# Performance work log

Hardware: AMD Instinct MI355X
Metric: run time of the kernel (lower is better)

## Reference

```python
import jax, jax.numpy as jnp
import numpy as np

N_NODES = 50000
N_EDGES = 800000
IN_C, HID_C, OUT_C = 256, 256, 128


def gcn_conv(x, W, b, row, col, n_nodes):
    """PyG GCNConv: linear transform, symmetric-normalized aggregation, bias.
    row/col already include self-loops. Messages flow row -> col."""
    h = x @ W  # [N, out]
    deg = jax.ops.segment_sum(jnp.ones_like(col, dtype=h.dtype), col, num_segments=n_nodes)
    d_inv_sqrt = jnp.where(deg > 0, jax.lax.rsqrt(jnp.maximum(deg, 1e-12)), 0.0)
    norm = d_inv_sqrt[row] * d_inv_sqrt[col]  # [E]
    msg = h[row] * norm[:, None]              # gather + scale, [E, out]
    out = jax.ops.segment_sum(msg, col, num_segments=n_nodes)  # scatter-add
    return out + b


def setup_inputs() -> dict:
    key = jax.random.key(0)
    k_x, k_e, k_w1, k_w2 = jax.random.split(key, 4)
    x = jax.random.normal(k_x, (N_NODES, IN_C), dtype=jnp.float32)
    edge_index = jax.random.randint(k_e, (2, N_EDGES), 0, N_NODES, dtype=jnp.int64)
    # Glorot-style init for GCN weights, zeros bias (PyG default)
    s1 = float(np.sqrt(6.0 / (IN_C + HID_C)))
    s2 = float(np.sqrt(6.0 / (HID_C + OUT_C)))
    W1 = jax.random.uniform(k_w1, (IN_C, HID_C), dtype=jnp.float32, minval=-s1, maxval=s1)
    b1 = jnp.zeros((HID_C,), dtype=jnp.float32)
    W2 = jax.random.uniform(k_w2, (HID_C, OUT_C), dtype=jnp.float32, minval=-s2, maxval=s2)
    b2 = jnp.zeros((OUT_C,), dtype=jnp.float32)
    return {"x": x, "edge_index": edge_index, "W1": W1, "b1": b1, "W2": W2, "b2": b2}


def reference(x, edge_index, W1, b1, W2, b2):
    n = x.shape[0]
    # add self-loops (PyG GCNConv default add_self_loops=True)
    loops = jnp.arange(n, dtype=edge_index.dtype)
    row = jnp.concatenate([edge_index[0], loops])
    col = jnp.concatenate([edge_index[1], loops])
    h = gcn_conv(x, W1, b1, row, col, n)
    h = jax.nn.relu(h)  # dropout p=0.0 -> identity
    out = gcn_conv(h, W2, b2, row, col, n)
    return out
```

## Files before the change

### kernel.cpp

```cpp
#include <hip/hip_runtime.h>

#define NN 50000
#define NE 800000
#define IN_C 256
#define HID_C 256
#define OUT_C 128

typedef unsigned short u16;
typedef __attribute__((ext_vector_type(8))) short short8;
typedef __attribute__((ext_vector_type(8))) unsigned short ushort8;
typedef __attribute__((ext_vector_type(4))) float f32x4;

__device__ __forceinline__ u16 f2b(float f) {
  unsigned int u = __float_as_uint(f);
  return (u16)((u + 0x7FFFu + ((u >> 16) & 1u)) >> 16);
}
__device__ __forceinline__ float b2f(u16 s) {
  return __uint_as_float(((unsigned int)s) << 16);
}


__global__ __launch_bounds__(256) void hist_kernel(const int* __restrict__ col,
                                                   int* __restrict__ cnt, int E) {
  int e = blockIdx.x * blockDim.x + threadIdx.x;
  if (e < E) atomicAdd(&cnt[col[e]], 1);
}

__global__ __launch_bounds__(256) void scan1_kernel(const int* __restrict__ cnt,
                                                    int* __restrict__ bsum, int n) {
  __shared__ int ws[4];
  int i = blockIdx.x * 256 + threadIdx.x;
  int lane = threadIdx.x & 63, wid = threadIdx.x >> 6;
  int v = (i < n) ? cnt[i] : 0;
#pragma unroll
  for (int off = 32; off > 0; off >>= 1) v += __shfl_down(v, off, 64);
  if (lane == 0) ws[wid] = v;
  __syncthreads();
  if (threadIdx.x == 0) bsum[blockIdx.x] = ws[0] + ws[1] + ws[2] + ws[3];
}

__global__ __launch_bounds__(256) void scan2_kernel(const int* __restrict__ bsum,
                                                    int* __restrict__ boff,
                                                    int* __restrict__ row_off,
                                                    int nb, int n) {
  __shared__ int wsum[4], wpre[5];
  int lane = threadIdx.x & 63, wid = threadIdx.x >> 6;
  int v = (threadIdx.x < nb) ? bsum[threadIdx.x] : 0;
  int s = v;
#pragma unroll
  for (int off = 1; off < 64; off <<= 1) {
    int t = __shfl_up(s, off, 64);
    if (lane >= off) s += t;
  }
  if (lane == 63) wsum[wid] = s;
  __syncthreads();
  if (threadIdx.x == 0) {
    int acc = 0;
#pragma unroll
    for (int w = 0; w < 4; ++w) { wpre[w] = acc; acc += wsum[w]; }
    wpre[4] = acc;
  }
  __syncthreads();
  if (threadIdx.x < nb) boff[threadIdx.x] = wpre[wid] + (s - v);
  if (threadIdx.x == 0) row_off[n] = wpre[4];
}

__global__ __launch_bounds__(256) void scan3_kernel(const int* __restrict__ cnt,
                                                    const int* __restrict__ boff,
                                                    int* __restrict__ row_off,
                                                    int* __restrict__ cursor,
                                                    float* __restrict__ dinv, int n) {
  __shared__ int wsum[4], wpre[4];
  int i = blockIdx.x * 256 + threadIdx.x;
  int lane = threadIdx.x & 63, wid = threadIdx.x >> 6;
  int v = (i < n) ? cnt[i] : 0;
  int s = v;
#pragma unroll
  for (int off = 1; off < 64; off <<= 1) {
    int t = __shfl_up(s, off, 64);
    if (lane >= off) s += t;
  }
  if (lane == 63) wsum[wid] = s;
  __syncthreads();
  if (threadIdx.x == 0) {
    int acc = 0;
#pragma unroll
    for (int w = 0; w < 4; ++w) { wpre[w] = acc; acc += wsum[w]; }
  }
  __syncthreads();
  if (i < n) {
    int off = boff[blockIdx.x] + wpre[wid] + (s - v);
    row_off[i] = off;
    cursor[i] = off;
    dinv[i] = rsqrtf((float)(v + 1));
  }
}

__global__ __launch_bounds__(256) void scatter_kernel(const int* __restrict__ row,
                                                      const int* __restrict__ col,
                                                      const float* __restrict__ dinv,
                                                      int* __restrict__ cursor,
                                                      int2* __restrict__ csr, int E) {
  int e = blockIdx.x * blockDim.x + threadIdx.x;
  if (e < E) {
    int r = row[e], c = col[e];
    int p = atomicAdd(&cursor[c], 1);
    csr[p] = make_int2(r, __float_as_int(dinv[r] * dinv[c]));
  }
}


__global__ __launch_bounds__(256) void convw_kernel(const float* __restrict__ W1,
                                                    const float* __restrict__ W2,
                                                    u16* __restrict__ W1t,
                                                    u16* __restrict__ W2t) {
  int id = blockIdx.x * 256 + threadIdx.x;
  if (id < 256 * 256) {
    int n = id >> 8, k = id & 255;
    W1t[id] = f2b(W1[k * 256 + n]);
  }
  if (id < 128 * 256) {
    int n = id >> 8, k = id & 255;
    W2t[id] = f2b(W2[k * 128 + n]);
  }
}


template <bool A_IS_F32>
__global__ __launch_bounds__(256) void gemm_mfma(const void* __restrict__ Ap,
                                                 const u16* __restrict__ Bt,
                                                 u16* __restrict__ C, int M, int N) {
  __shared__ u16 Asl[2][128 * 40];
  __shared__ u16 Bsl[2][128 * 40];
  const int tid = threadIdx.x;
  const int row0 = blockIdx.y * 128;
  const int col0 = blockIdx.x * 128;

  f32x4 acc[4][4] = {};

  const int seg = tid & 7;
  const int rb = tid >> 3;
  const int wave = tid >> 6, lane = tid & 63;
  const int wm = wave >> 1, wn = wave & 1;
  const int qr = lane & 15, quad = lane >> 4;

  float4 aF[4];
  ushort4 aU[4];
  ushort4 bR[4];

  auto load_tiles = [&](int k0) {
    if constexpr (A_IS_F32) {
      const float* A = (const float*)Ap;
#pragma unroll
      for (int i = 0; i < 4; ++i) {
        int gr = row0 + rb + i * 32;
        aF[i] = (gr < M) ? *(const float4*)&A[(size_t)gr * 256 + k0 + seg * 4]
                         : make_float4(0.f, 0.f, 0.f, 0.f);
      }
    } else {
      const u16* A = (const u16*)Ap;
#pragma unroll
      for (int i = 0; i < 4; ++i) {
        int gr = row0 + rb + i * 32;
        aU[i] = (gr < M) ? *(const ushort4*)&A[(size_t)gr * 256 + k0 + seg * 4]
                         : make_ushort4(0, 0, 0, 0);
      }
    }
#pragma unroll
    for (int i = 0; i < 4; ++i) {
      int n = rb + i * 32;
      bR[i] = *(const ushort4*)&Bt[(size_t)(col0 + n) * 256 + k0 + seg * 4];
    }
  };

  auto write_lds = [&](int buf) {
#pragma unroll
    for (int i = 0; i < 4; ++i) {
      int r = rb + i * 32;
      ushort4 u;
      if constexpr (A_IS_F32) {
        u.x = f2b(aF[i].x); u.y = f2b(aF[i].y);
        u.z = f2b(aF[i].z); u.w = f2b(aF[i].w);
      } else {
        u = aU[i];
      }
      *(ushort4*)&Asl[buf][r * 40 + seg * 4] = u;
      *(ushort4*)&Bsl[buf][r * 40 + seg * 4] = bR[i];
    }
  };

  load_tiles(0);
  write_lds(0);
  __syncthreads();

#pragma unroll
  for (int it = 0; it < 8; ++it) {
    const int cur = it & 1;
    if (it < 7) load_tiles((it + 1) * 32);

    short8 afr[4], bfr[4];
#pragma unroll
    for (int mt = 0; mt < 4; ++mt)
      afr[mt] = *(const short8*)&Asl[cur][(wm * 64 + mt * 16 + qr) * 40 + quad * 8];
#pragma unroll
    for (int nt = 0; nt < 4; ++nt)
      bfr[nt] = *(const short8*)&Bsl[cur][(wn * 64 + nt * 16 + qr) * 40 + quad * 8];
#pragma unroll
    for (int mt = 0; mt < 4; ++mt)
#pragma unroll
      for (int nt = 0; nt < 4; ++nt)
        acc[mt][nt] = __builtin_amdgcn_mfma_f32_16x16x32_bf16(afr[mt], bfr[nt], acc[mt][nt], 0, 0, 0);

    if (it < 7) {
      write_lds(1 - cur);
      __syncthreads();
    }
  }

#pragma unroll
  for (int mt = 0; mt < 4; ++mt) {
#pragma unroll
    for (int nt = 0; nt < 4; ++nt) {
      int gc = col0 + wn * 64 + nt * 16 + qr;
#pragma unroll
      for (int i = 0; i < 4; ++i) {
        int gr = row0 + wm * 64 + mt * 16 + quad * 4 + i;
        if (gr < M) C[(size_t)gr * N + gc] = f2b(acc[mt][nt][i]);
      }
    }
  }
}


__global__ __launch_bounds__(256) void agg256_bf(const u16* __restrict__ h,
                                                 const int* __restrict__ row_off,
                                                 const int2* __restrict__ csr,
                                                 const float* __restrict__ dinv,
                                                 const float* __restrict__ bias,
                                                 u16* __restrict__ out, int n) {
  int wave = threadIdx.x >> 6;
  int lane = threadIdx.x & 63;
  int half = lane >> 5;
  int sl = lane & 31;
  int v = blockIdx.x * 8 + wave * 2 + half;
  if (v >= n) return;
  int beg = row_off[v], end = row_off[v + 1];
  float a[8] = {};
  int e = beg;
  for (; e + 3 < end; e += 4) {
    int2 e0 = csr[e], e1 = csr[e + 1], e2 = csr[e + 2], e3 = csr[e + 3];
    ushort8 h0 = *(const ushort8*)&h[(size_t)e0.x * 256 + sl * 8];
    ushort8 h1 = *(const ushort8*)&h[(size_t)e1.x * 256 + sl * 8];
    ushort8 h2 = *(const ushort8*)&h[(size_t)e2.x * 256 + sl * 8];
    ushort8 h3 = *(const ushort8*)&h[(size_t)e3.x * 256 + sl * 8];
    float w0 = __int_as_float(e0.y), w1 = __int_as_float(e1.y);
    float w2 = __int_as_float(e2.y), w3 = __int_as_float(e3.y);
#pragma unroll
    for (int i = 0; i < 8; ++i)
      a[i] += b2f((u16)h0[i]) * w0 + b2f((u16)h1[i]) * w1 +
              b2f((u16)h2[i]) * w2 + b2f((u16)h3[i]) * w3;
  }
  for (; e < end; ++e) {
    int2 e0 = csr[e];
    ushort8 h0 = *(const ushort8*)&h[(size_t)e0.x * 256 + sl * 8];
    float w0 = __int_as_float(e0.y);
#pragma unroll
    for (int i = 0; i < 8; ++i) a[i] += b2f((u16)h0[i]) * w0;
  }
  float dv = dinv[v];
  float sw = dv * dv;
  ushort8 hs = *(const ushort8*)&h[(size_t)v * 256 + sl * 8];
  float4 bv0 = *(const float4*)&bias[sl * 8];
  float4 bv1 = *(const float4*)&bias[sl * 8 + 4];
  float bb[8] = {bv0.x, bv0.y, bv0.z, bv0.w, bv1.x, bv1.y, bv1.z, bv1.w};
  ushort8 o;
#pragma unroll
  for (int i = 0; i < 8; ++i) {
    float r = fmaxf(a[i] + b2f((u16)hs[i]) * sw + bb[i], 0.f);
    o[i] = (short)f2b(r);
  }
  *(ushort8*)&out[(size_t)v * 256 + sl * 8] = o;
}

__global__ __launch_bounds__(256) void agg128_bf(const u16* __restrict__ h,
                                                 const int* __restrict__ row_off,
                                                 const int2* __restrict__ csr,
                                                 const float* __restrict__ dinv,
                                                 const float* __restrict__ bias,
                                                 float* __restrict__ out, int n) {
  int wave = threadIdx.x >> 6;
  int lane = threadIdx.x & 63;
  int quarter = lane >> 4;
  int sl = lane & 15;
  int v = blockIdx.x * 16 + wave * 4 + quarter;
  if (v >= n) return;
  int beg = row_off[v], end = row_off[v + 1];
  float a[8] = {};
  int e = beg;
  for (; e + 3 < end; e += 4) {
    int2 e0 = csr[e], e1 = csr[e + 1], e2 = csr[e + 2], e3 = csr[e + 3];
    ushort8 h0 = *(const ushort8*)&h[(size_t)e0.x * 128 + sl * 8];
    ushort8 h1 = *(const ushort8*)&h[(size_t)e1.x * 128 + sl * 8];
    ushort8 h2 = *(const ushort8*)&h[(size_t)e2.x * 128 + sl * 8];
    ushort8 h3 = *(const ushort8*)&h[(size_t)e3.x * 128 + sl * 8];
    float w0 = __int_as_float(e0.y), w1 = __int_as_float(e1.y);
    float w2 = __int_as_float(e2.y), w3 = __int_as_float(e3.y);
#pragma unroll
    for (int i = 0; i < 8; ++i)
      a[i] += b2f((u16)h0[i]) * w0 + b2f((u16)h1[i]) * w1 +
              b2f((u16)h2[i]) * w2 + b2f((u16)h3[i]) * w3;
  }
  for (; e < end; ++e) {
    int2 e0 = csr[e];
    ushort8 h0 = *(const ushort8*)&h[(size_t)e0.x * 128 + sl * 8];
    float w0 = __int_as_float(e0.y);
#pragma unroll
    for (int i = 0; i < 8; ++i) a[i] += b2f((u16)h0[i]) * w0;
  }
  float dv = dinv[v];
  float sw = dv * dv;
  ushort8 hs = *(const ushort8*)&h[(size_t)v * 128 + sl * 8];
  float4 bv0 = *(const float4*)&bias[sl * 8];
  float4 bv1 = *(const float4*)&bias[sl * 8 + 4];
  float bb[8] = {bv0.x, bv0.y, bv0.z, bv0.w, bv1.x, bv1.y, bv1.z, bv1.w};
  float o[8];
#pragma unroll
  for (int i = 0; i < 8; ++i) o[i] = a[i] + b2f((u16)hs[i]) * sw + bb[i];
  *(float4*)&out[(size_t)v * 128 + sl * 8] = make_float4(o[0], o[1], o[2], o[3]);
  *(float4*)&out[(size_t)v * 128 + sl * 8 + 4] = make_float4(o[4], o[5], o[6], o[7]);
}


extern "C" void kernel_launch(void* const* d_in, const int* in_sizes, int n_in,
                              void* d_out, int out_size, void* d_ws, size_t ws_size,
                              hipStream_t stream) {
  const float* x = (const float*)d_in[0];
  const int* ei = (const int*)d_in[1];
  const float* W1 = (const float*)d_in[2];
  const float* b1 = (const float*)d_in[3];
  const float* W2 = (const float*)d_in[4];
  const float* b2 = (const float*)d_in[5];
  float* out = (float*)d_out;

  const int* row = ei;
  const int* col = ei + NE;

  const int NB = (NN + 255) / 256;

  u16* Hb = (u16*)d_ws;
  u16* H2b = Hb + (size_t)NN * 256;
  u16* H3b = H2b + (size_t)NN * 256;
  u16* W1t = H3b + (size_t)NN * 128;
  u16* W2t = W1t + 256 * 256;
  int* cnt = (int*)(W2t + 128 * 256);
  int* row_off = cnt + NN;
  int* cursor = row_off + NN + 1;
  float* dinv = (float*)(cursor + NN);
  int* bsum = (int*)(dinv + NN);
  int* boff = bsum + NB;
  int2* csr = (int2*)(boff + NB);

  hipMemsetAsync(cnt, 0, NN * sizeof(int), stream);
  convw_kernel<<<256, 256, 0, stream>>>(W1, W2, W1t, W2t);
  hist_kernel<<<(NE + 255) / 256, 256, 0, stream>>>(col, cnt, NE);
  scan1_kernel<<<NB, 256, 0, stream>>>(cnt, bsum, NN);
  scan2_kernel<<<1, 256, 0, stream>>>(bsum, boff, row_off, NB, NN);
  scan3_kernel<<<NB, 256, 0, stream>>>(cnt, boff, row_off, cursor, dinv, NN);
  scatter_kernel<<<(NE + 255) / 256, 256, 0, stream>>>(row, col, dinv, cursor, csr, NE);

  {
    dim3 grid(HID_C / 128, (NN + 127) / 128);
    gemm_mfma<true><<<grid, 256, 0, stream>>>(x, W1t, Hb, NN, HID_C);
  }
  agg256_bf<<<(NN + 7) / 8, 256, 0, stream>>>(Hb, row_off, csr, dinv, b1, H2b, NN);

  {
    dim3 grid(OUT_C / 128, (NN + 127) / 128);
    gemm_mfma<false><<<grid, 256, 0, stream>>>(H2b, W2t, H3b, NN, OUT_C);
  }
  agg128_bf<<<(NN + 15) / 16, 256, 0, stream>>>(H3b, row_off, csr, dinv, b2, out, NN);
}
```

Measured before the change: 307.7 us.

## Fold symmetric normalization into GEMM epilogue and store source-only CSR

The d^-1/2 factor of the source node is now applied to each row in the GEMM epilogue, and the destination factor is applied once per node after aggregation. The CSR therefore holds only source indices (int instead of int2), and the aggregation loop becomes a plain sum. That loop is also unrolled to 8 gathers in flight to expose more memory parallelism. This halves CSR traffic and removes per-edge multiplies, at the cost of a per-row dinv load in the GEMM epilogue and more registers in the aggregation kernels.

```diff
diff --git a/kernel.cpp b/kernel.cpp
--- a/kernel.cpp
+++ b/kernel.cpp
@@ -98,14 +98,13 @@
 
 __global__ __launch_bounds__(256) void scatter_kernel(const int* __restrict__ row,
                                                       const int* __restrict__ col,
-                                                      const float* __restrict__ dinv,
                                                       int* __restrict__ cursor,
-                                                      int2* __restrict__ csr, int E) {
+                                                      int* __restrict__ csr, int E) {
   int e = blockIdx.x * blockDim.x + threadIdx.x;
   if (e < E) {
-    int r = row[e], c = col[e];
+    int c = col[e];
     int p = atomicAdd(&cursor[c], 1);
-    csr[p] = make_int2(r, __float_as_int(dinv[r] * dinv[c]));
+    csr[p] = row[e];
   }
 }
 
@@ -129,6 +128,7 @@
 template <bool A_IS_F32>
 __global__ __launch_bounds__(256) void gemm_mfma(const void* __restrict__ Ap,
                                                  const u16* __restrict__ Bt,
+                                                 const float* __restrict__ dscale,
                                                  u16* __restrict__ C, int M, int N) {
   __shared__ u16 Asl[2][128 * 40];
   __shared__ u16 Bsl[2][128 * 40];
@@ -220,12 +220,15 @@
 #pragma unroll
   for (int mt = 0; mt < 4; ++mt) {
 #pragma unroll
-    for (int nt = 0; nt < 4; ++nt) {
-      int gc = col0 + wn * 64 + nt * 16 + qr;
-#pragma unroll
-      for (int i = 0; i < 4; ++i) {
-        int gr = row0 + wm * 64 + mt * 16 + quad * 4 + i;
-        if (gr < M) C[(size_t)gr * N + gc] = f2b(acc[mt][nt][i]);
+    for (int i = 0; i < 4; ++i) {
+      int gr = row0 + wm * 64 + mt * 16 + quad * 4 + i;
+      if (gr < M) {
+        float sc = dscale[gr];
+#pragma unroll
+        for (int nt = 0; nt < 4; ++nt) {
+          int gc = col0 + wn * 64 + nt * 16 + qr;
+          C[(size_t)gr * N + gc] = f2b(acc[mt][nt][i] * sc);
+        }
       }
     }
   }
@@ -234,7 +237,7 @@
 
 __global__ __launch_bounds__(256) void agg256_bf(const u16* __restrict__ h,
                                                  const int* __restrict__ row_off,
-                                                 const int2* __restrict__ csr,
+                                                 const int* __restrict__ csr,
                                                  const float* __restrict__ dinv,
                                                  const float* __restrict__ bias,
                                                  u16* __restrict__ out, int n) {
@@ -247,36 +250,43 @@
   int beg = row_off[v], end = row_off[v + 1];
   float a[8] = {};
   int e = beg;
-  for (; e + 3 < end; e += 4) {
-    int2 e0 = csr[e], e1 = csr[e + 1], e2 = csr[e + 2], e3 = csr[e + 3];
-    ushort8 h0 = *(const ushort8*)&h[(size_t)e0.x * 256 + sl * 8];
-    ushort8 h1 = *(const ushort8*)&h[(size_t)e1.x * 256 + sl * 8];
-    ushort8 h2 = *(const ushort8*)&h[(size_t)e2.x * 256 + sl * 8];
-    ushort8 h3 = *(const ushort8*)&h[(size_t)e3.x * 256 + sl * 8];
-    float w0 = __int_as_float(e0.y), w1 = __int_as_float(e1.y);
-    float w2 = __int_as_float(e2.y), w3 = __int_as_float(e3.y);
-#pragma unroll
-    for (int i = 0; i < 8; ++i)
-      a[i] += b2f((u16)h0[i]) * w0 + b2f((u16)h1[i]) * w1 +
-              b2f((u16)h2[i]) * w2 + b2f((u16)h3[i]) * w3;
-  }
-  for (; e < end; ++e) {
-    int2 e0 = csr[e];
-    ushort8 h0 = *(const ushort8*)&h[(size_t)e0.x * 256 + sl * 8];
-    float w0 = __int_as_float(e0.y);
-#pragma unroll
-    for (int i = 0; i < 8; ++i) a[i] += b2f((u16)h0[i]) * w0;
-  }
+  for (; e + 7 < end; e += 8) {
+    int s[8];
+#pragma unroll
+    for (int j = 0; j < 8; ++j) s[j] = csr[e + j];
+    ushort8 g[8];
+#pragma unroll
+    for (int j = 0; j < 8; ++j)
+      g[j] = *(const ushort8*)&h[(size_t)s[j] * 256 + sl * 8];
+#pragma unroll
+    for (int j = 0; j < 8; ++j)
+#pragma unroll
+      for (int i = 0; i < 8; ++i) a[i] += b2f((u16)g[j][i]);
+  }
+  for (; e + 1 < end; e += 2) {
+    int s0 = csr[e], s1 = csr[e + 1];
+    ushort8 g0 = *(const ushort8*)&h[(size_t)s0 * 256 + sl * 8];
+    ushort8 g1 = *(const ushort8*)&h[(size_t)s1 * 256 + sl * 8];
+#pragma unroll
+    for (int i = 0; i < 8; ++i) a[i] += b2f((u16)g0[i]) + b2f((u16)g1[i]);
+  }
+  if (e < end) {
+    int s0 = csr[e];
+    ushort8 g0 = *(const ushort8*)&h[(size_t)s0 * 256 + sl * 8];
+#pragma unroll
+    for (int i = 0; i < 8; ++i) a[i] += b2f((u16)g0[i]);
+  }
+  ushort8 hs = *(const ushort8*)&h[(size_t)v * 256 + sl * 8];
+#pragma unroll
+  for (int i = 0; i < 8; ++i) a[i] += b2f((u16)hs[i]);
   float dv = dinv[v];
-  float sw = dv * dv;
-  ushort8 hs = *(const ushort8*)&h[(size_t)v * 256 + sl * 8];
   float4 bv0 = *(const float4*)&bias[sl * 8];
   float4 bv1 = *(const float4*)&bias[sl * 8 + 4];
   float bb[8] = {bv0.x, bv0.y, bv0.z, bv0.w, bv1.x, bv1.y, bv1.z, bv1.w};
   ushort8 o;
 #pragma unroll
   for (int i = 0; i < 8; ++i) {
-    float r = fmaxf(a[i] + b2f((u16)hs[i]) * sw + bb[i], 0.f);
+    float r = fmaxf(a[i] * dv + bb[i], 0.f);
     o[i] = (short)f2b(r);
   }
   *(ushort8*)&out[(size_t)v * 256 + sl * 8] = o;
@@ -284,7 +294,7 @@
 
 __global__ __launch_bounds__(256) void agg128_bf(const u16* __restrict__ h,
                                                  const int* __restrict__ row_off,
-                                                 const int2* __restrict__ csr,
+                                                 const int* __restrict__ csr,
                                                  const float* __restrict__ dinv,
                                                  const float* __restrict__ bias,
                                                  float* __restrict__ out, int n) {
@@ -297,35 +307,42 @@
   int beg = row_off[v], end = row_off[v + 1];
   float a[8] = {};
   int e = beg;
-  for (; e + 3 < end; e += 4) {
-    int2 e0 = csr[e], e1 = csr[e + 1], e2 = csr[e + 2], e3 = csr[e + 3];
-    ushort8 h0 = *(const ushort8*)&h[(size_t)e0.x * 128 + sl * 8];
-    ushort8 h1 = *(const ushort8*)&h[(size_t)e1.x * 128 + sl * 8];
-    ushort8 h2 = *(const ushort8*)&h[(size_t)e2.x * 128 + sl * 8];
-    ushort8 h3 = *(const ushort8*)&h[(size_t)e3.x * 128 + sl * 8];
-    float w0 = __int_as_float(e0.y), w1 = __int_as_float(e1.y);
-    float w2 = __int_as_float(e2.y), w3 = __int_as_float(e3.y);
-#pragma unroll
-    for (int i = 0; i < 8; ++i)
-      a[i] += b2f((u16)h0[i]) * w0 + b2f((u16)h1[i]) * w1 +
-              b2f((u16)h2[i]) * w2 + b2f((u16)h3[i]) * w3;
-  }
-  for (; e < end; ++e) {
-    int2 e0 = csr[e];
-    ushort8 h0 = *(const ushort8*)&h[(size_t)e0.x * 128 + sl * 8];
-    float w0 = __int_as_float(e0.y);
-#pragma unroll
-    for (int i = 0; i < 8; ++i) a[i] += b2f((u16)h0[i]) * w0;
-  }
+  for (; e + 7 < end; e += 8) {
+    int s[8];
+#pragma unroll
+    for (int j = 0; j < 8; ++j) s[j] = csr[e + j];
+    ushort8 g[8];
+#pragma unroll
+    for (int j = 0; j < 8; ++j)
+      g[j] = *(const ushort8*)&h[(size_t)s[j] * 128 + sl * 8];
+#pragma unroll
+    for (int j = 0; j < 8; ++j)
+#pragma unroll
+      for (int i = 0; i < 8; ++i) a[i] += b2f((u16)g[j][i]);
+  }
+  for (; e + 1 < end; e += 2) {
+    int s0 = csr[e], s1 = csr[e + 1];
+    ushort8 g0 = *(const ushort8*)&h[(size_t)s0 * 128 + sl * 8];
+    ushort8 g1 = *(const ushort8*)&h[(size_t)s1 * 128 + sl * 8];
+#pragma unroll
+    for (int i = 0; i < 8; ++i) a[i] += b2f((u16)g0[i]) + b2f((u16)g1[i]);
+  }
+  if (e < end) {
+    int s0 = csr[e];
+    ushort8 g0 = *(const ushort8*)&h[(size_t)s0 * 128 + sl * 8];
+#pragma unroll
+    for (int i = 0; i < 8; ++i) a[i] += b2f((u16)g0[i]);
+  }
+  ushort8 hs = *(const ushort8*)&h[(size_t)v * 128 + sl * 8];
+#pragma unroll
+  for (int i = 0; i < 8; ++i) a[i] += b2f((u16)hs[i]);
   float dv = dinv[v];
-  float sw = dv * dv;
-  ushort8 hs = *(const ushort8*)&h[(size_t)v * 128 + sl * 8];
   float4 bv0 = *(const float4*)&bias[sl * 8];
   float4 bv1 = *(const float4*)&bias[sl * 8 + 4];
   float bb[8] = {bv0.x, bv0.y, bv0.z, bv0.w, bv1.x, bv1.y, bv1.z, bv1.w};
   float o[8];
 #pragma unroll
-  for (int i = 0; i < 8; ++i) o[i] = a[i] + b2f((u16)hs[i]) * sw + bb[i];
+  for (int i = 0; i < 8; ++i) o[i] = a[i] * dv + bb[i];
   *(float4*)&out[(size_t)v * 128 + sl * 8] = make_float4(o[0], o[1], o[2], o[3]);
   *(float4*)&out[(size_t)v * 128 + sl * 8 + 4] = make_float4(o[4], o[5], o[6], o[7]);
 }
@@ -358,7 +375,7 @@
   float* dinv = (float*)(cursor + NN);
   int* bsum = (int*)(dinv + NN);
   int* boff = bsum + NB;
-  int2* csr = (int2*)(boff + NB);
+  int* csr = boff + NB;
 
   hipMemsetAsync(cnt, 0, NN * sizeof(int), stream);
   convw_kernel<<<256, 256, 0, stream>>>(W1, W2, W1t, W2t);
@@ -366,17 +383,17 @@
   scan1_kernel<<<NB, 256, 0, stream>>>(cnt, bsum, NN);
   scan2_kernel<<<1, 256, 0, stream>>>(bsum, boff, row_off, NB, NN);
   scan3_kernel<<<NB, 256, 0, stream>>>(cnt, boff, row_off, cursor, dinv, NN);
-  scatter_kernel<<<(NE + 255) / 256, 256, 0, stream>>>(row, col, dinv, cursor, csr, NE);
+  scatter_kernel<<<(NE + 255) / 256, 256, 0, stream>>>(row, col, cursor, csr, NE);
 
   {
     dim3 grid(HID_C / 128, (NN + 127) / 128);
-    gemm_mfma<true><<<grid, 256, 0, stream>>>(x, W1t, Hb, NN, HID_C);
+    gemm_mfma<true><<<grid, 256, 0, stream>>>(x, W1t, dinv, Hb, NN, HID_C);
   }
   agg256_bf<<<(NN + 7) / 8, 256, 0, stream>>>(Hb, row_off, csr, dinv, b1, H2b, NN);
 
   {
     dim3 grid(OUT_C / 128, (NN + 127) / 128);
-    gemm_mfma<false><<<grid, 256, 0, stream>>>(H2b, W2t, H3b, NN, OUT_C);
+    gemm_mfma<false><<<grid, 256, 0, stream>>>(H2b, W2t, dinv, H3b, NN, OUT_C);
   }
   agg128_bf<<<(NN + 15) / 16, 256, 0, stream>>>(H3b, row_off, csr, dinv, b2, out, NN);
 }
```

Measured after the change: 316.7 us. 2.9% more time.
